# Performance work log

Hardware: AMD Instinct MI355X
Metric: run time of the kernel (lower is better)

The kernel has to match this reference:

```python
import jax, jax.numpy as jnp
import numpy as np

EMBED_DIM = 1024
NUM_HEADS = 16
HEAD_DIM = EMBED_DIM // NUM_HEADS
VOCAB = 5          # languages
BOTTLENECK = 800
SCALING = HEAD_DIM ** -0.5


def setup_inputs() -> dict:
    key = jax.random.key(0)
    ks = jax.random.split(key, 16)
    T, B, D = 2048, 2, EMBED_DIM
    s = 0.02
    return {
        "query": jax.random.normal(ks[0], (T, B, D), jnp.float32),
        "key": jax.random.normal(ks[1], (T, B, D), jnp.float32),
        "value": jax.random.normal(ks[2], (T, B, D), jnp.float32),
        "wq": jax.random.normal(ks[3], (D, D), jnp.float32) * s,
        "bq": jnp.zeros((D,), jnp.float32),
        "wk": jax.random.normal(ks[4], (D, D), jnp.float32) * s,
        "bk": jnp.zeros((D,), jnp.float32),
        "wv": jax.random.normal(ks[5], (D, D), jnp.float32) * s,
        "bv": jnp.zeros((D,), jnp.float32),
        "wo": jax.random.normal(ks[6], (D, D), jnp.float32) * s,
        "bo": jnp.zeros((D,), jnp.float32),
        "wte": jax.random.normal(ks[7], (VOCAB, D), jnp.float32) * s,
        "ct_w1": jax.random.normal(ks[8], (VOCAB, BOTTLENECK, D), jnp.float32) * s,
        "ct_b1": jnp.zeros((VOCAB, BOTTLENECK), jnp.float32),
        "ct_w2": jax.random.normal(ks[9], (VOCAB, 2 * D, BOTTLENECK), jnp.float32) * s,
        "ct_b2": jnp.zeros((VOCAB, 2 * D), jnp.float32),
        "language_id": jax.random.randint(ks[10], (B,), 0, VOCAB, jnp.int32),
    }


def _prefix_kv(language_id, wte, ct_w1, ct_b1, ct_w2, ct_b2):
    # PrefixTuningLangEmbLangspec: embed lang id, run all 5 bottleneck MLPs,
    # select per-sample MLP output via one-hot weighting, split into K/V.
    B = language_id.shape[0]
    emb = wte[language_id]                                  # [B, D]
    h = jnp.tanh(jnp.einsum("bd,chd->cbh", emb, ct_w1) + ct_b1[:, None, :])  # [5,B,800]
    kv = jnp.einsum("cbh,cdh->cbd", h, ct_w2) + ct_b2[:, None, :]            # [5,B,2D]
    w = jax.nn.one_hot(language_id, VOCAB, dtype=kv.dtype)  # [B,5]
    kv_sel = jnp.einsum("bc,cbd->bd", w, kv)                # [B,2D]
    # view(b,1,2,nh,hd): first D -> keys, second D -> values
    pk = kv_sel[:, :EMBED_DIM].reshape(B, NUM_HEADS, 1, HEAD_DIM)
    pv = kv_sel[:, EMBED_DIM:].reshape(B, NUM_HEADS, 1, HEAD_DIM)
    return pk, pv


def reference(query, key, value, wq, bq, wk, bk, wv, bv, wo, bo,
              wte, ct_w1, ct_b1, ct_w2, ct_b2, language_id):
    T, B, D = query.shape
    pk, pv = _prefix_kv(language_id, wte, ct_w1, ct_b1, ct_w2, ct_b2)  # [B,H,1,hd]

    # separate Q/K/V projections (Linear: x @ W^T + b)
    q = (jnp.einsum("tbd,ed->tbe", query, wq) + bq) * SCALING
    k = jnp.einsum("tbd,ed->tbe", key, wk) + bk
    v = jnp.einsum("tbd,ed->tbe", value, wv) + bv

    # [T,B,D] -> [B,H,T,hd]
    def split_heads(x):
        return x.reshape(T, B, NUM_HEADS, HEAD_DIM).transpose(1, 2, 0, 3)

    qh = split_heads(q)
    kh = jnp.concatenate([pk, split_heads(k)], axis=2)  # [B,H,T+1,hd]
    vh = jnp.concatenate([pv, split_heads(v)], axis=2)

    scores = jnp.einsum("bhqd,bhkd->bhqk", qh, kh)      # [B,H,T,T+1]
    attn = jax.nn.softmax(scores, axis=-1)
    ctx = jnp.einsum("bhqk,bhkd->bhqd", attn, vh)       # [B,H,T,hd]

    ctx = ctx.transpose(2, 0, 1, 3).reshape(T, B, D)    # back to [T,B,D]
    out = jnp.einsum("tbd,ed->tbe", ctx, wo) + bo
    return out
```

## Files before the change

kernel.cpp:

```cpp
#include <hip/hip_runtime.h>
#include <stdint.h>

#define T_SEQ 2048
#define BATCH 2
#define DIM   1024
#define NH    16
#define HD    64
#define TKP   2112

typedef _Float16 v8h __attribute__((ext_vector_type(8)));
typedef _Float16 v4h __attribute__((ext_vector_type(4)));
typedef float    f32x4 __attribute__((ext_vector_type(4)));

__device__ __forceinline__ void gload16(const _Float16* g, _Float16* l) {
  __builtin_amdgcn_global_load_lds(
      (__attribute__((address_space(1))) unsigned int*)g,
      (__attribute__((address_space(3))) unsigned int*)l, 16, 0, 0);
}

__global__ void cvt_all(const float4* __restrict__ s0, const float4* __restrict__ s1,
                        const float4* __restrict__ s2, const float4* __restrict__ s3,
                        const float4* __restrict__ s4, const float4* __restrict__ s5,
                        const float4* __restrict__ s6,
                        v4h* __restrict__ d0, v4h* __restrict__ d1, v4h* __restrict__ d2,
                        v4h* __restrict__ d3, v4h* __restrict__ d4, v4h* __restrict__ d5,
                        v4h* __restrict__ d6) {
  const int NTB4 = 1048576, DD4 = 262144;
  int i = blockIdx.x * 256 + threadIdx.x;
  const float4* s; v4h* d; int off;
  if (i < 3 * NTB4) {
    int t = i / NTB4; off = i - t * NTB4;
    s = t == 0 ? s0 : t == 1 ? s1 : s2;
    d = t == 0 ? d0 : t == 1 ? d1 : d2;
  } else {
    int j = i - 3 * NTB4;
    int t = j / DD4; off = j - t * DD4;
    s = t == 0 ? s3 : t == 1 ? s4 : t == 2 ? s5 : s6;
    d = t == 0 ? d3 : t == 1 ? d4 : t == 2 ? d5 : d6;
  }
  float4 v = s[off];
  v4h o = { (_Float16)v.x, (_Float16)v.y, (_Float16)v.z, (_Float16)v.w };
  d[off] = o;
}

__global__ void prefix_h_k(const float* __restrict__ wte, const float* __restrict__ w1,
                           const float* __restrict__ b1, const int* __restrict__ lang,
                           float* __restrict__ hbuf) {
  int wid = blockIdx.x * 4 + (threadIdx.x >> 6);
  int lane = threadIdx.x & 63;
  int b = wid / 800, j = wid - b * 800;
  int c = lang[b];
  const float* wr = w1 + ((size_t)c * 800 + j) * 1024;
  const float* em = wte + (size_t)c * 1024;
  float s = 0.f;
  for (int d = lane; d < 1024; d += 64) s += wr[d] * em[d];
  for (int off = 32; off > 0; off >>= 1) s += __shfl_down(s, off, 64);
  if (lane == 0) hbuf[wid] = tanhf(s + b1[c * 800 + j]);
}

__global__ void prefix_kv_k(const float* __restrict__ w2, const float* __restrict__ b2,
                            const float* __restrict__ hbuf, const int* __restrict__ lang,
                            _Float16* __restrict__ kb, _Float16* __restrict__ vb) {
  int wid = blockIdx.x * 4 + (threadIdx.x >> 6);
  int lane = threadIdx.x & 63;
  int b = wid >> 11, e = wid & 2047;
  int c = lang[b];
  const float* wr = w2 + ((size_t)c * 2048 + e) * 800;
  const float* hb = hbuf + b * 800;
  float s = 0.f;
  for (int j = lane; j < 800; j += 64) s += wr[j] * hb[j];
  for (int off = 32; off > 0; off >>= 1) s += __shfl_down(s, off, 64);
  if (lane == 0) {
    float val = s + b2[c * 2048 + e];
    if (e < 1024) {
      int h = e >> 6, hd = e & 63;
      kb[((size_t)(b * 16 + h) * TKP + 2048) * 64 + hd] = (_Float16)val;
    } else {
      int d = e - 1024;
      int h = d >> 6, hd = d & 63;
      vb[((size_t)(b * 16 + h) * 64 + hd) * TKP + 2048] = (_Float16)val;
    }
  }
}

__global__ void pad_k(_Float16* kb, _Float16* vb) {
  int bh = blockIdx.x;
  v8h z = {};
  _Float16* kp = kb + ((size_t)bh * TKP + 2048) * 64;
  for (int i = threadIdx.x; i < 512; i += 256) *(v8h*)&kp[i * 8] = z;
  for (int i = threadIdx.x; i < 512; i += 256) {
    int c = i >> 3, seg = i & 7;
    *(v8h*)&vb[((size_t)bh * 64 + c) * TKP + 2048 + seg * 8] = z;
  }
}

__global__ __launch_bounds__(256) void gemm_bt_k(
    const _Float16* __restrict__ A0, const _Float16* __restrict__ A1, const _Float16* __restrict__ A2,
    const _Float16* __restrict__ W0, const _Float16* __restrict__ W1, const _Float16* __restrict__ W2,
    const float* __restrict__ bs0, const float* __restrict__ bs1, const float* __restrict__ bs2,
    _Float16* __restrict__ qb, _Float16* __restrict__ kb, _Float16* __restrict__ vb,
    float* __restrict__ fout, int mode_base)
{
  __shared__ __align__(16) _Float16 smem[128 * 64 * 2];
  _Float16* As = smem;
  _Float16* Bs = smem + 128 * 64;
  const int mode = mode_base + blockIdx.z;
  const _Float16* A = (mode == 1) ? A1 : (mode == 2) ? A2 : A0;
  const _Float16* W = (mode == 1) ? W1 : (mode == 2) ? W2 : W0;
  const float* bias = (mode == 1) ? bs1 : (mode == 2) ? bs2 : bs0;
  const int tid = threadIdx.x, w = tid >> 6, lane = tid & 63;
  const int quad = lane >> 4, l15 = lane & 15;
  const int r0 = blockIdx.x * 128, c0 = blockIdx.y * 128;
  const int wm = w >> 1, wn = w & 1;
  const int srow = lane >> 3, sseg = lane & 7;
  f32x4 acc[4][4] = {};
  for (int k0 = 0; k0 < 1024; k0 += 64) {
    for (int i = 0; i < 4; ++i) {
      int rowb = w * 32 + i * 8;
      gload16(A + (size_t)(r0 + rowb + srow) * 1024 + k0 + sseg * 8, &As[rowb * 64]);
      gload16(W + (size_t)(c0 + rowb + srow) * 1024 + k0 + sseg * 8, &Bs[rowb * 64]);
    }
    __syncthreads();
    for (int ks = 0; ks < 2; ++ks) {
      v8h af[4], bfr[4];
      for (int mt = 0; mt < 4; ++mt)
        af[mt] = *(const v8h*)&As[(wm * 64 + mt * 16 + l15) * 64 + ks * 32 + quad * 8];
      for (int nt = 0; nt < 4; ++nt)
        bfr[nt] = *(const v8h*)&Bs[(wn * 64 + nt * 16 + l15) * 64 + ks * 32 + quad * 8];
      for (int mt = 0; mt < 4; ++mt)
        for (int nt = 0; nt < 4; ++nt)
          acc[mt][nt] = __builtin_amdgcn_mfma_f32_16x16x32_f16(af[mt], bfr[nt], acc[mt][nt], 0, 0, 0);
    }
    __syncthreads();
  }
  if (mode == 3) {
    for (int nt = 0; nt < 4; ++nt) {
      int e = c0 + wn * 64 + nt * 16 + l15;
      float be = bias[e];
      for (int mt = 0; mt < 4; ++mt) {
        int rb = r0 + wm * 64 + mt * 16 + quad * 4;
        for (int reg = 0; reg < 4; ++reg)
          fout[(size_t)(rb + reg) * 1024 + e] = acc[mt][nt][reg] + be;
      }
    }
    return;
  }
  _Float16* st = smem + w * 4096;
  const float qscale = (mode == 0) ? 0.125f : 1.0f;
  for (int p = 0; p < 2; ++p) {
    __syncthreads();
    for (int ntl = 0; ntl < 2; ++ntl) {
      int nt = p * 2 + ntl;
      int e = c0 + wn * 64 + nt * 16 + l15;
      float be = bias[e];
      for (int mt = 0; mt < 4; ++mt)
        for (int reg = 0; reg < 4; ++reg) {
          float val = (acc[mt][nt][reg] + be) * qscale;
          int rl = mt * 16 + quad * 4 + reg;
          if (mode != 2) st[rl * 40 + ntl * 16 + l15] = (_Float16)val;
          else st[(ntl * 16 + l15) * 72 + (rl & 1) * 32 + (rl >> 1)] = (_Float16)val;
        }
    }
    __syncthreads();
    if (mode != 2) {
      for (int it = 0; it < 4; ++it) {
        int chunk = it * 64 + lane;
        int rr = chunk >> 2, seg = chunk & 3;
        v8h val = *(const v8h*)&st[rr * 40 + seg * 8];
        int r = r0 + wm * 64 + rr, b = r & 1, t = r >> 1;
        int e0 = c0 + wn * 64 + p * 32 + seg * 8;
        int h = e0 >> 6, hd0 = e0 & 63;
        if (mode == 0) *(v8h*)&qb[((size_t)(b * 16 + h) * 2048 + t) * 64 + hd0] = val;
        else           *(v8h*)&kb[((size_t)(b * 16 + h) * TKP + t) * 64 + hd0] = val;
      }
    } else {
      for (int it = 0; it < 4; ++it) {
        int chunk = it * 64 + lane;
        int el = chunk >> 3, b = (chunk >> 2) & 1, qs = chunk & 3;
        v8h val = *(const v8h*)&st[el * 72 + b * 32 + qs * 8];
        int e = c0 + wn * 64 + p * 32 + el;
        int h = e >> 6, hd = e & 63;
        int t0 = ((r0 + wm * 64) >> 1) + qs * 8;
        *(v8h*)&vb[((size_t)(b * 16 + h) * 64 + hd) * TKP + t0] = val;
      }
    }
  }
}

__global__ __launch_bounds__(256) void attn_k(
    const _Float16* __restrict__ qb, const _Float16* __restrict__ kb,
    const _Float16* __restrict__ vb, _Float16* __restrict__ ctx)
{
  __shared__ __align__(16) _Float16 Qs[128 * 72];
  __shared__ __align__(16) _Float16 Ks[64 * 72];
  __shared__ __align__(16) _Float16 Vs[64 * 72];
  __shared__ __align__(16) _Float16 Ps[128 * 72];
  const int bh = blockIdx.x;
  const int qt0 = blockIdx.y * 128;
  const int tid = threadIdx.x, w = tid >> 6, lane = tid & 63;
  const int quad = lane >> 4, l15 = lane & 15;
  for (int it = 0; it < 4; ++it) {
    int slot = it * 256 + tid;
    int row = slot >> 3, seg = slot & 7;
    int4 v = *(const int4*)(qb + ((size_t)bh * 2048 + qt0 + row) * 64 + seg * 8);
    *(int4*)&Qs[row * 72 + seg * 8] = v;
  }
  const int sr = tid >> 3, sseg = tid & 7;
  const _Float16* kptr = kb + (size_t)bh * TKP * 64 + sr * 64 + sseg * 8;
  const _Float16* vptr = vb + (size_t)bh * 64 * TKP + (size_t)sr * TKP + sseg * 8;
  int4 kp0 = *(const int4*)kptr, kp1 = *(const int4*)(kptr + 2048);
  int4 vp0 = *(const int4*)vptr, vp1 = *(const int4*)(vptr + 32 * TKP);
  kptr += 4096; vptr += 64;
  f32x4 O[4][2] = {};
  float l_[2] = { 0.f, 0.f };
  for (int kc = 0; kc < 33; ++kc) {
    __syncthreads();
    *(int4*)&Ks[sr * 72 + sseg * 8] = kp0;
    *(int4*)&Ks[(sr + 32) * 72 + sseg * 8] = kp1;
    *(int4*)&Vs[sr * 72 + sseg * 8] = vp0;
    *(int4*)&Vs[(sr + 32) * 72 + sseg * 8] = vp1;
    __syncthreads();
    if (kc < 32) {
      kp0 = *(const int4*)kptr; kp1 = *(const int4*)(kptr + 2048);
      vp0 = *(const int4*)vptr; vp1 = *(const int4*)(vptr + 32 * TKP);
      kptr += 4096; vptr += 64;
    }
    f32x4 S[4][2] = {};
    for (int ks = 0; ks < 2; ++ks) {
      v8h q0 = *(const v8h*)&Qs[(w * 32 + l15) * 72 + ks * 32 + quad * 8];
      v8h q1 = *(const v8h*)&Qs[(w * 32 + 16 + l15) * 72 + ks * 32 + quad * 8];
      for (int mt = 0; mt < 4; ++mt) {
        v8h ak = *(const v8h*)&Ks[(mt * 16 + l15) * 72 + ks * 32 + quad * 8];
        S[mt][0] = __builtin_amdgcn_mfma_f32_16x16x32_f16(ak, q0, S[mt][0], 0, 0, 0);
        S[mt][1] = __builtin_amdgcn_mfma_f32_16x16x32_f16(ak, q1, S[mt][1], 0, 0, 0);
      }
    }
    if (kc == 32) {
      for (int mt = 0; mt < 4; ++mt)
        for (int reg = 0; reg < 4; ++reg)
          if (mt * 16 + quad * 4 + reg > 0) { S[mt][0][reg] = -1e30f; S[mt][1][reg] = -1e30f; }
    }
    for (int nt = 0; nt < 2; ++nt) {
      float rsum = 0.f;
      for (int mt = 0; mt < 4; ++mt) {
        float p0 = __expf(S[mt][nt][0]);
        float p1 = __expf(S[mt][nt][1]);
        float p2 = __expf(S[mt][nt][2]);
        float p3 = __expf(S[mt][nt][3]);
        rsum += (p0 + p1) + (p2 + p3);
        v4h pk4 = { (_Float16)p0, (_Float16)p1, (_Float16)p2, (_Float16)p3 };
        *(v4h*)&Ps[(w * 32 + nt * 16 + l15) * 72 + mt * 16 + quad * 4] = pk4;
      }
      l_[nt] += rsum;
    }
    for (int ks = 0; ks < 2; ++ks) {
      v8h p0 = *(const v8h*)&Ps[(w * 32 + l15) * 72 + ks * 32 + quad * 8];
      v8h p1 = *(const v8h*)&Ps[(w * 32 + 16 + l15) * 72 + ks * 32 + quad * 8];
      for (int ht = 0; ht < 4; ++ht) {
        v8h av = *(const v8h*)&Vs[(ht * 16 + l15) * 72 + ks * 32 + quad * 8];
        O[ht][0] = __builtin_amdgcn_mfma_f32_16x16x32_f16(av, p0, O[ht][0], 0, 0, 0);
        O[ht][1] = __builtin_amdgcn_mfma_f32_16x16x32_f16(av, p1, O[ht][1], 0, 0, 0);
      }
    }
  }
  for (int nt = 0; nt < 2; ++nt) {
    l_[nt] += __shfl_xor(l_[nt], 16, 64);
    l_[nt] += __shfl_xor(l_[nt], 32, 64);
  }
  const int b = bh >> 4, hh = bh & 15;
  for (int nt = 0; nt < 2; ++nt) {
    float inv = 1.f / l_[nt];
    int q = qt0 + w * 32 + nt * 16 + l15;
    for (int ht = 0; ht < 4; ++ht) {
      v4h o4 = { (_Float16)(O[ht][nt][0] * inv), (_Float16)(O[ht][nt][1] * inv),
                 (_Float16)(O[ht][nt][2] * inv), (_Float16)(O[ht][nt][3] * inv) };
      *(v4h*)(ctx + ((size_t)q * 2 + b) * 1024 + hh * 64 + ht * 16 + quad * 4) = o4;
    }
  }
}

extern "C" void kernel_launch(void* const* d_in, const int* in_sizes, int n_in,
                              void* d_out, int out_size, void* d_ws, size_t ws_size,
                              hipStream_t stream) {
  (void)in_sizes; (void)n_in; (void)out_size; (void)ws_size;
  const float* query = (const float*)d_in[0];
  const float* key_  = (const float*)d_in[1];
  const float* value = (const float*)d_in[2];
  const float* wq = (const float*)d_in[3];
  const float* bq = (const float*)d_in[4];
  const float* wk = (const float*)d_in[5];
  const float* bk = (const float*)d_in[6];
  const float* wv = (const float*)d_in[7];
  const float* bv = (const float*)d_in[8];
  const float* wo = (const float*)d_in[9];
  const float* bo = (const float*)d_in[10];
  const float* wte = (const float*)d_in[11];
  const float* w1 = (const float*)d_in[12];
  const float* b1 = (const float*)d_in[13];
  const float* w2 = (const float*)d_in[14];
  const float* b2 = (const float*)d_in[15];
  const int* lang = (const int*)d_in[16];
  float* out = (float*)d_out;

  const size_t NTB = (size_t)T_SEQ * BATCH * DIM;
  const size_t DD  = (size_t)DIM * DIM;
  const size_t KVN = (size_t)BATCH * NH * TKP * HD;
  _Float16* xq  = (_Float16*)d_ws;
  _Float16* xk  = xq + NTB;
  _Float16* xv  = xk + NTB;
  _Float16* wqb = xv + NTB;
  _Float16* wkb = wqb + DD;
  _Float16* wvb = wkb + DD;
  _Float16* wob = wvb + DD;
  _Float16* qbuf = wob + DD;
  _Float16* kbuf = qbuf + NTB;
  _Float16* vbuf = kbuf + KVN;
  float* hbuf = (float*)(vbuf + KVN);
  _Float16* ctxb = xq;

  cvt_all<<<16384, 256, 0, stream>>>((const float4*)query, (const float4*)key_,
                                     (const float4*)value, (const float4*)wq,
                                     (const float4*)wk, (const float4*)wv, (const float4*)wo,
                                     (v4h*)xq, (v4h*)xk, (v4h*)xv, (v4h*)wqb,
                                     (v4h*)wkb, (v4h*)wvb, (v4h*)wob);
  pad_k<<<32, 256, 0, stream>>>(kbuf, vbuf);
  prefix_h_k<<<400, 256, 0, stream>>>(wte, w1, b1, lang, hbuf);
  prefix_kv_k<<<1024, 256, 0, stream>>>(w2, b2, hbuf, lang, kbuf, vbuf);
  gemm_bt_k<<<dim3(32, 8, 3), 256, 0, stream>>>(xq, xk, xv, wqb, wkb, wvb, bq, bk, bv,
                                                qbuf, kbuf, vbuf, nullptr, 0);
  attn_k<<<dim3(32, 16), 256, 0, stream>>>(qbuf, kbuf, vbuf, ctxb);
  gemm_bt_k<<<dim3(32, 8, 1), 256, 0, stream>>>(ctxb, ctxb, ctxb, wob, wob, wob, bo, bo, bo,
                                                qbuf, kbuf, vbuf, out, 3);
}
```

Baseline: 307.9 us.

## Hold Q in registers, use exp2 and MFMA row sums in attention

New measurement: 318.6 us. +3.5%, slower.

```diff
diff --git a/kernel.cpp b/kernel.cpp
--- a/kernel.cpp
+++ b/kernel.cpp
@@ -10,6 +10,8 @@
 
 typedef _Float16 v8h __attribute__((ext_vector_type(8)));
 typedef _Float16 v4h __attribute__((ext_vector_type(4)));
+typedef _Float16 v2h __attribute__((ext_vector_type(2)));
+typedef __fp16   pk2 __attribute__((ext_vector_type(2)));
 typedef float    f32x4 __attribute__((ext_vector_type(4)));
 
 __device__ __forceinline__ void gload16(const _Float16* g, _Float16* l) {
@@ -146,7 +148,7 @@
     return;
   }
   _Float16* st = smem + w * 4096;
-  const float qscale = (mode == 0) ? 0.125f : 1.0f;
+  const float qscale = (mode == 0) ? 0.125f * 1.44269504f : 1.0f;
   for (int p = 0; p < 2; ++p) {
     __syncthreads();
     for (int ntl = 0; ntl < 2; ++ntl) {
@@ -187,14 +189,15 @@
   }
 }
 
-__global__ __launch_bounds__(256) void attn_k(
+__global__ __launch_bounds__(256, 4) void attn_k(
     const _Float16* __restrict__ qb, const _Float16* __restrict__ kb,
     const _Float16* __restrict__ vb, _Float16* __restrict__ ctx)
 {
-  __shared__ __align__(16) _Float16 Qs[128 * 72];
-  __shared__ __align__(16) _Float16 Ks[64 * 72];
-  __shared__ __align__(16) _Float16 Vs[64 * 72];
-  __shared__ __align__(16) _Float16 Ps[128 * 72];
+  __shared__ __align__(16) _Float16 smem[18432];
+  _Float16* Ks = smem;
+  _Float16* Vs = smem + 4608;
+  _Float16* Ps = smem + 9216;
+  _Float16* Qstage = smem;
   const int bh = blockIdx.x;
   const int qt0 = blockIdx.y * 128;
   const int tid = threadIdx.x, w = tid >> 6, lane = tid & 63;
@@ -203,16 +206,23 @@
     int slot = it * 256 + tid;
     int row = slot >> 3, seg = slot & 7;
     int4 v = *(const int4*)(qb + ((size_t)bh * 2048 + qt0 + row) * 64 + seg * 8);
-    *(int4*)&Qs[row * 72 + seg * 8] = v;
-  }
+    *(int4*)&Qstage[row * 72 + seg * 8] = v;
+  }
+  __syncthreads();
+  v8h qf[2][2];
+  for (int nt = 0; nt < 2; ++nt)
+    for (int ks = 0; ks < 2; ++ks)
+      qf[nt][ks] = *(const v8h*)&Qstage[(w * 32 + nt * 16 + l15) * 72 + ks * 32 + quad * 8];
   const int sr = tid >> 3, sseg = tid & 7;
   const _Float16* kptr = kb + (size_t)bh * TKP * 64 + sr * 64 + sseg * 8;
   const _Float16* vptr = vb + (size_t)bh * 64 * TKP + (size_t)sr * TKP + sseg * 8;
   int4 kp0 = *(const int4*)kptr, kp1 = *(const int4*)(kptr + 2048);
   int4 vp0 = *(const int4*)vptr, vp1 = *(const int4*)(vptr + 32 * TKP);
   kptr += 4096; vptr += 64;
+  const _Float16 h1 = (_Float16)1.f;
+  const v8h ones = { h1, h1, h1, h1, h1, h1, h1, h1 };
   f32x4 O[4][2] = {};
-  float l_[2] = { 0.f, 0.f };
+  f32x4 Lacc[2] = {};
   for (int kc = 0; kc < 33; ++kc) {
     __syncthreads();
     *(int4*)&Ks[sr * 72 + sseg * 8] = kp0;
@@ -226,36 +236,33 @@
       kptr += 4096; vptr += 64;
     }
     f32x4 S[4][2] = {};
-    for (int ks = 0; ks < 2; ++ks) {
-      v8h q0 = *(const v8h*)&Qs[(w * 32 + l15) * 72 + ks * 32 + quad * 8];
-      v8h q1 = *(const v8h*)&Qs[(w * 32 + 16 + l15) * 72 + ks * 32 + quad * 8];
+    for (int ks = 0; ks < 2; ++ks)
       for (int mt = 0; mt < 4; ++mt) {
         v8h ak = *(const v8h*)&Ks[(mt * 16 + l15) * 72 + ks * 32 + quad * 8];
-        S[mt][0] = __builtin_amdgcn_mfma_f32_16x16x32_f16(ak, q0, S[mt][0], 0, 0, 0);
-        S[mt][1] = __builtin_amdgcn_mfma_f32_16x16x32_f16(ak, q1, S[mt][1], 0, 0, 0);
-      }
-    }
+        S[mt][0] = __builtin_amdgcn_mfma_f32_16x16x32_f16(ak, qf[0][ks], S[mt][0], 0, 0, 0);
+        S[mt][1] = __builtin_amdgcn_mfma_f32_16x16x32_f16(ak, qf[1][ks], S[mt][1], 0, 0, 0);
+      }
     if (kc == 32) {
       for (int mt = 0; mt < 4; ++mt)
         for (int reg = 0; reg < 4; ++reg)
           if (mt * 16 + quad * 4 + reg > 0) { S[mt][0][reg] = -1e30f; S[mt][1][reg] = -1e30f; }
     }
-    for (int nt = 0; nt < 2; ++nt) {
-      float rsum = 0.f;
+    for (int nt = 0; nt < 2; ++nt)
       for (int mt = 0; mt < 4; ++mt) {
-        float p0 = __expf(S[mt][nt][0]);
-        float p1 = __expf(S[mt][nt][1]);
-        float p2 = __expf(S[mt][nt][2]);
-        float p3 = __expf(S[mt][nt][3]);
-        rsum += (p0 + p1) + (p2 + p3);
-        v4h pk4 = { (_Float16)p0, (_Float16)p1, (_Float16)p2, (_Float16)p3 };
+        float p0 = exp2f(S[mt][nt][0]);
+        float p1 = exp2f(S[mt][nt][1]);
+        float p2 = exp2f(S[mt][nt][2]);
+        float p3 = exp2f(S[mt][nt][3]);
+        v2h lo = __builtin_bit_cast(v2h, __builtin_amdgcn_cvt_pkrtz(p0, p1));
+        v2h hi = __builtin_bit_cast(v2h, __builtin_amdgcn_cvt_pkrtz(p2, p3));
+        v4h pk4 = __builtin_shufflevector(lo, hi, 0, 1, 2, 3);
         *(v4h*)&Ps[(w * 32 + nt * 16 + l15) * 72 + mt * 16 + quad * 4] = pk4;
       }
-      l_[nt] += rsum;
-    }
     for (int ks = 0; ks < 2; ++ks) {
       v8h p0 = *(const v8h*)&Ps[(w * 32 + l15) * 72 + ks * 32 + quad * 8];
       v8h p1 = *(const v8h*)&Ps[(w * 32 + 16 + l15) * 72 + ks * 32 + quad * 8];
+      Lacc[0] = __builtin_amdgcn_mfma_f32_16x16x32_f16(ones, p0, Lacc[0], 0, 0, 0);
+      Lacc[1] = __builtin_amdgcn_mfma_f32_16x16x32_f16(ones, p1, Lacc[1], 0, 0, 0);
       for (int ht = 0; ht < 4; ++ht) {
         v8h av = *(const v8h*)&Vs[(ht * 16 + l15) * 72 + ks * 32 + quad * 8];
         O[ht][0] = __builtin_amdgcn_mfma_f32_16x16x32_f16(av, p0, O[ht][0], 0, 0, 0);
@@ -263,13 +270,9 @@
       }
     }
   }
-  for (int nt = 0; nt < 2; ++nt) {
-    l_[nt] += __shfl_xor(l_[nt], 16, 64);
-    l_[nt] += __shfl_xor(l_[nt], 32, 64);
-  }
   const int b = bh >> 4, hh = bh & 15;
   for (int nt = 0; nt < 2; ++nt) {
-    float inv = 1.f / l_[nt];
+    float inv = 1.f / Lacc[nt][0];
     int q = qt0 + w * 32 + nt * 16 + l15;
     for (int ht = 0; ht < 4; ++ht) {
       v4h o4 = { (_Float16)(O[ht][nt][0] * inv), (_Float16)(O[ht][nt][1] * inv),
```
